# Performance work log

Hardware: AMD Instinct MI355X
Metric: run time of the kernel (lower is better)

## Reference

```python
import jax, jax.numpy as jnp
import numpy as np
import math

HIDDEN = 2048
HEADS = 16
HEAD_DIM = HIDDEN // HEADS
MAX_SEQ = 4096
ROPE_BASE = 10000.0


def rope_cos_sin(seq_len):
    # (seq_len, head_dim//2) angle table
    inv_freq = 1.0 / (ROPE_BASE ** (jnp.arange(0, HEAD_DIM, 2, dtype=jnp.float32) / HEAD_DIM))
    t = jnp.arange(seq_len, dtype=jnp.float32)
    ang = jnp.einsum('s,f->sf', t, inv_freq)
    return jnp.cos(ang), jnp.sin(ang)


def apply_rope(x, cos, sin):
    # x: (b, s, h, d); interleaved complex pairs along last dim
    b, s, h, d = x.shape
    xr = x.reshape(b, s, h, d // 2, 2)
    x0, x1 = xr[..., 0], xr[..., 1]
    c = cos[:s][None, :, None, :]
    sn = sin[:s][None, :, None, :]
    o0 = x0 * c - x1 * sn
    o1 = x0 * sn + x1 * c
    return jnp.stack([o0, o1], axis=-1).reshape(b, s, h, d)


def setup_inputs() -> dict:
    key = jax.random.key(0)
    k1, k2, k3, k4, k5, k6 = jax.random.split(key, 6)
    B, SQ, SK = 2, 2048, 2048
    x = jax.random.normal(k1, (B, SQ, HIDDEN), dtype=jnp.float32)
    enc = jax.random.normal(k2, (B, SK, HIDDEN), dtype=jnp.float32)
    mask = jnp.ones((B, SK), dtype=jnp.int32)
    scale = 0.02
    Wq = jax.random.normal(k3, (HIDDEN, HIDDEN), dtype=jnp.float32) * scale
    Wk = jax.random.normal(k4, (HIDDEN, HIDDEN), dtype=jnp.float32) * scale
    Wv = jax.random.normal(k5, (HIDDEN, HIDDEN), dtype=jnp.float32) * scale
    Wo = jax.random.normal(k6, (HIDDEN, HIDDEN), dtype=jnp.float32) * scale
    return {"x": x, "encoder_output": enc, "encoder_attention_mask": mask,
            "Wq": Wq, "Wk": Wk, "Wv": Wv, "Wo": Wo}


def reference(x, encoder_output, encoder_attention_mask, Wq, Wk, Wv, Wo):
    B, SQ, _ = x.shape
    SK = encoder_output.shape[1]
    # nn.Linear(bias=False): y = x @ W^T
    q = (x @ Wq.T).reshape(B, SQ, HEADS, HEAD_DIM)
    k = (encoder_output @ Wk.T).reshape(B, SK, HEADS, HEAD_DIM)
    v = (encoder_output @ Wv.T).reshape(B, SK, HEADS, HEAD_DIM)
    cos, sin = rope_cos_sin(max(SQ, SK))
    q = apply_rope(q, cos, sin)
    k = apply_rope(k, cos, sin)
    scale = math.sqrt(HEAD_DIM)
    # (b, h, sq, sk) scores
    scores = jnp.einsum('bqhd,bkhd->bhqk', q, k) / scale
    mask = encoder_attention_mask[:, None, None, :]
    scores = jnp.where(mask == 0, -jnp.inf, scores)
    attn = jax.nn.softmax(scores, axis=-1)
    out = jnp.einsum('bhqk,bkhd->bqhd', attn, v).reshape(B, SQ, HIDDEN)
    return out @ Wo.T
```

## Files before the change

### kernel.cpp

```cpp
#include <hip/hip_runtime.h>
#include <stdint.h>


#define LOG2E 1.44269504088896340736f
#define INV2PI 0.15915494309189535f

typedef __attribute__((ext_vector_type(8))) short bf16x8;
typedef __attribute__((ext_vector_type(8))) uint16_t u16x8;
typedef __attribute__((ext_vector_type(4))) uint16_t u16x4;
typedef __attribute__((ext_vector_type(4))) float f32x4;

__device__ __forceinline__ uint16_t f2bf(float f) {
  union { float f; uint32_t i; } v; v.f = f;
  uint32_t x = v.i;
  return (uint16_t)((x + 0x7fffu + ((x >> 16) & 1u)) >> 16);
}
__device__ __forceinline__ uint32_t f_as_u(float f) { union { float f; uint32_t u; } v; v.f = f; return v.u; }
__device__ __forceinline__ float u_as_f(uint32_t u) { union { uint32_t u; float f; } v; v.u = u; return v.f; }
__device__ __forceinline__ void glds16(const void* g, void* l) {
  __builtin_amdgcn_global_load_lds((const __attribute__((address_space(1))) void*)g,
                                   (__attribute__((address_space(3))) void*)l, 16, 0, 0);
}

__global__ __launch_bounds__(256) void convert_f32_bf16(const float* __restrict__ in,
                                                        uint16_t* __restrict__ out) {
  const long i = ((long)blockIdx.x * 256 + threadIdx.x) * 8;
  const f32x4 a = *(const f32x4*)(in + i);
  const f32x4 b = *(const f32x4*)(in + i + 4);
  u16x8 o;
#pragma unroll
  for (int j = 0; j < 4; ++j) { o[j] = f2bf(a[j]); o[4 + j] = f2bf(b[j]); }
  *(u16x8*)(out + i) = o;
}

__global__ __launch_bounds__(256) void mask_bias(const int* __restrict__ m,
                                                 float* __restrict__ bias) {
  const int i = blockIdx.x * 256 + threadIdx.x;
  bias[i] = m[i] ? 0.0f : -__builtin_inff();
}

#define EPI_ROPE 0
#define EPI_VT   1
#define EPI_F32  2

template <int MODE>
__global__ __launch_bounds__(256) void gemm_bt(const uint16_t* __restrict__ A,
                                               const uint16_t* __restrict__ W,
                                               void* __restrict__ Cv,
                                               int M, int N, int K, float oscale) {
  __shared__ __align__(16) uint16_t As[128 * 32];
  __shared__ __align__(16) uint16_t Bs[128 * 32];
  const int tid = threadIdx.x;
  const int lane = tid & 63;
  const int w = tid >> 6;
  const int r16 = lane & 15, quad = lane >> 4;
  const int m0 = blockIdx.y * 128, n0 = blockIdx.x * 128;
  const int wm = (w >> 1) * 64, wn = (w & 1) * 64;
  f32x4 acc[4][4] = {};
  const int srow = 32 * w + (lane >> 2);
  const int scol = (lane & 3) * 8;
  const uint16_t* Ag = A + (long)(m0 + srow) * K + scol;
  const uint16_t* Wg = W + (long)(n0 + srow) * K + scol;
  uint16_t* AsW = As + 2 * w * 512;
  uint16_t* BsW = Bs + 2 * w * 512;
  for (int k0 = 0; k0 < K; k0 += 32) {
    glds16(Ag + k0, AsW);
    glds16(Ag + k0 + (long)16 * K, AsW + 512);
    glds16(Wg + k0, BsW);
    glds16(Wg + k0 + (long)16 * K, BsW + 512);
    __syncthreads();
    bf16x8 af[4], bfr[4];
#pragma unroll
    for (int mt = 0; mt < 4; ++mt)
      af[mt] = *(const bf16x8*)(As + (wm + mt * 16 + r16) * 32 + quad * 8);
#pragma unroll
    for (int nt = 0; nt < 4; ++nt)
      bfr[nt] = *(const bf16x8*)(Bs + (wn + nt * 16 + r16) * 32 + quad * 8);
#pragma unroll
    for (int mt = 0; mt < 4; ++mt)
#pragma unroll
      for (int nt = 0; nt < 4; ++nt)
        acc[mt][nt] = __builtin_amdgcn_mfma_f32_16x16x32_bf16(af[mt], bfr[nt], acc[mt][nt], 0, 0, 0);
    __syncthreads();
  }

#pragma unroll
  for (int mt = 0; mt < 4; ++mt)
#pragma unroll
    for (int nt = 0; nt < 4; ++nt) {
      const int col = n0 + wn + nt * 16 + r16;
      const int rowbase = m0 + wm + mt * 16 + quad * 4;
      if constexpr (MODE == EPI_F32) {
        float* C = (float*)Cv;
#pragma unroll
        for (int r = 0; r < 4; ++r)
          C[(long)(rowbase + r) * N + col] = acc[mt][nt][r];
      } else if constexpr (MODE == EPI_ROPE) {
        uint16_t* C = (uint16_t*)Cv;
        const int f = (col >> 1) & 63;
        const float inv = __builtin_amdgcn_exp2f((float)f * (-13.287712379549449f / 64.0f));
        const float sgn = (col & 1) ? 1.0f : -1.0f;
#pragma unroll
        for (int r = 0; r < 4; ++r) {
          const float val = acc[mt][nt][r];
          const float partner = __shfl_xor(val, 1);
          const int s = (rowbase + r) & 2047;
          const float rev = __builtin_amdgcn_fractf((float)s * inv * INV2PI);
          const float sn = __builtin_amdgcn_sinf(rev);
          const float cs = __builtin_amdgcn_cosf(rev);
          C[(long)(rowbase + r) * N + col] = f2bf((val * cs + sgn * partner * sn) * oscale);
        }
      } else {
        uint16_t* Vt = (uint16_t*)Cv;
        const int h = col >> 7, d = col & 127;
        const int b = rowbase >> 11, s = rowbase & 2047;
        u16x4 pk;
#pragma unroll
        for (int r = 0; r < 4; ++r) pk[r] = f2bf(acc[mt][nt][r]);
        *(u16x4*)(Vt + (long)((b * 16 + h) * 128 + d) * 2048 + s) = pk;
      }
    }
}

__global__ __launch_bounds__(256) void attn_kernel(const uint16_t* __restrict__ Q,
                                                   const uint16_t* __restrict__ K,
                                                   const uint16_t* __restrict__ Vt,
                                                   const float* __restrict__ bias,
                                                   uint16_t* __restrict__ O) {
  __shared__ __align__(16) uint16_t Ks[2][32 * 128];
  __shared__ __align__(16) uint16_t Vts[2][128 * 32];
  __shared__ __align__(16) uint16_t Ps[4][32 * 40];
  const int tid = threadIdx.x;
  const int lane = tid & 63;
  const int w = tid >> 6;
  const int r16 = lane & 15, quad = lane >> 4;
  const int h = blockIdx.y, b = blockIdx.z;
  const int qbase = blockIdx.x * 128 + w * 32;

  bf16x8 qf[2][4];
#pragma unroll
  for (int t = 0; t < 2; ++t) {
    const uint16_t* qb = Q + ((long)(b * 2048 + qbase + t * 16 + r16)) * 2048 + h * 128 + quad * 8;
#pragma unroll
    for (int c = 0; c < 4; ++c) qf[t][c] = *(const bf16x8*)(qb + c * 32);
  }
  f32x4 oacc[2][8] = {};
  float li[2][4] = {};

  uint16_t* PsW = &Ps[w][0];
  const float* brow = bias + b * 2048;

  const int key0[2] = {8 * w + quad, 8 * w + 4 + quad};
  const uint16_t* kg[2];
  const uint16_t* vg[2];
#pragma unroll
  for (int i = 0; i < 2; ++i) {
    kg[i] = K + ((long)(b * 2048 + key0[i])) * 2048 + h * 128 + 8 * (r16 ^ ((4 * i + quad) & 7));
    const int dim = 32 * w + 16 * i + (lane >> 2);
    vg[i] = Vt + ((long)((b * 16 + h) * 128 + dim)) * 2048 + 8 * ((lane & 3) ^ ((lane >> 2) & 3));
  }

#pragma unroll
  for (int i = 0; i < 2; ++i) {
    glds16(kg[i], &Ks[0][(2 * w + i) * 512]);
    glds16(vg[i], &Vts[0][(2 * w + i) * 512]);
    kg[i] += 32 * 2048;
    vg[i] += 32;
  }
  float bn0 = brow[r16], bn1 = brow[16 + r16];

  auto body = [&](int k0, const uint16_t* Kc, const uint16_t* Vc,
                  uint16_t* Kn, uint16_t* Vn, bool pf) {
    __syncthreads();
    const float bc0 = bn0, bc1 = bn1;
    if (pf) {
#pragma unroll
      for (int i = 0; i < 2; ++i) {
        glds16(kg[i], Kn + (2 * w + i) * 512);
        glds16(vg[i], Vn + (2 * w + i) * 512);
        kg[i] += 32 * 2048;
        vg[i] += 32;
      }
      bn0 = brow[k0 + 32 + r16];
      bn1 = brow[k0 + 48 + r16];
    }
#pragma unroll
    for (int ct = 0; ct < 2; ++ct) {
      const int key = ct * 16 + r16;
      const int kb = key & 7;
      bf16x8 kf[4];
#pragma unroll
      for (int c = 0; c < 4; ++c)
        kf[c] = *(const bf16x8*)(Kc + key * 128 + ((4 * c + quad) ^ kb) * 8);
      const float bv = ct ? bc1 : bc0;
      const int pc = ct * 2 + (r16 >> 3);
#pragma unroll
      for (int t = 0; t < 2; ++t) {
        f32x4 s = {};
#pragma unroll
        for (int c = 0; c < 4; ++c)
          s = __builtin_amdgcn_mfma_f32_16x16x32_bf16(qf[t][c], kf[c], s, 0, 0, 0);
#pragma unroll
        for (int r = 0; r < 4; ++r) {
          const float p = __builtin_amdgcn_exp2f(s[r] + bv);
          const uint32_t pb = f_as_u(p) + 0x8000u;
          const int row = t * 16 + quad * 4 + r;
          PsW[row * 40 + ((pc ^ r) << 3) + (r16 & 7)] = (uint16_t)(pb >> 16);
          li[t][r] += u_as_f(pb & 0xffff0000u);
        }
      }
    }
    bf16x8 pa[2];
#pragma unroll
    for (int t = 0; t < 2; ++t)
      pa[t] = *(const bf16x8*)(PsW + (t * 16 + r16) * 40 + ((quad ^ (r16 & 3)) << 3));
#pragma unroll
    for (int nt = 0; nt < 8; ++nt) {
      const int dim = nt * 16 + r16;
      bf16x8 vf = *(const bf16x8*)(Vc + dim * 32 + ((quad ^ (dim & 3)) << 3));
#pragma unroll
      for (int t = 0; t < 2; ++t)
        oacc[t][nt] = __builtin_amdgcn_mfma_f32_16x16x32_bf16(pa[t], vf, oacc[t][nt], 0, 0, 0);
    }
  };

  for (int kt2 = 0; kt2 < 32; ++kt2) {
    body(64 * kt2,      &Ks[0][0], &Vts[0][0], &Ks[1][0], &Vts[1][0], true);
    body(64 * kt2 + 32, &Ks[1][0], &Vts[1][0], &Ks[0][0], &Vts[0][0], kt2 < 31);
  }

#pragma unroll
  for (int off = 1; off < 16; off <<= 1)
#pragma unroll
    for (int t = 0; t < 2; ++t)
#pragma unroll
      for (int r = 0; r < 4; ++r) li[t][r] += __shfl_xor(li[t][r], off);

#pragma unroll
  for (int t = 0; t < 2; ++t) {
    uint16_t* ob = O + ((long)(b * 2048 + qbase + t * 16)) * 2048 + h * 128;
    float inv_l[4];
#pragma unroll
    for (int r = 0; r < 4; ++r) inv_l[r] = 1.0f / li[t][r];
#pragma unroll
    for (int nt = 0; nt < 8; ++nt)
#pragma unroll
      for (int r = 0; r < 4; ++r)
        ob[(long)(quad * 4 + r) * 2048 + nt * 16 + r16] = f2bf(oacc[t][nt][r] * inv_l[r]);
  }
}

extern "C" void kernel_launch(void* const* d_in, const int* in_sizes, int n_in,
                              void* d_out, int out_size, void* d_ws, size_t ws_size,
                              hipStream_t stream) {
  const float* x   = (const float*)d_in[0];
  const float* enc = (const float*)d_in[1];
  const int*   msk = (const int*)d_in[2];
  const float* Wq  = (const float*)d_in[3];
  const float* Wk  = (const float*)d_in[4];
  const float* Wv  = (const float*)d_in[5];
  const float* Wo  = (const float*)d_in[6];
  float* out = (float*)d_out;

  const long NELT = 8L * 1024 * 1024;
  const long WELT = 4L * 1024 * 1024;
  uint16_t* Qb   = (uint16_t*)d_ws;
  uint16_t* Kb   = Qb + NELT;
  uint16_t* Vtb  = Kb + NELT;
  uint16_t* xb   = Vtb + NELT;
  uint16_t* encb = xb + NELT;
  uint16_t* Wb   = encb + NELT;
  uint16_t* Ob   = xb;
  float*    biasb = (float*)encb;

  const float cs_exp = 0.088388347648318447f * LOG2E;

  const dim3 gb(16, 32);
  const int CB_ACT = (int)(NELT / 2048);
  const int CB_W   = (int)(WELT / 2048);

  convert_f32_bf16<<<CB_ACT, 256, 0, stream>>>(x, xb);
  convert_f32_bf16<<<CB_W, 256, 0, stream>>>(Wq, Wb);
  gemm_bt<EPI_ROPE><<<gb, 256, 0, stream>>>(xb, Wb, Qb, 4096, 2048, 2048, cs_exp);

  convert_f32_bf16<<<CB_ACT, 256, 0, stream>>>(enc, encb);
  convert_f32_bf16<<<CB_W, 256, 0, stream>>>(Wk, Wb);
  gemm_bt<EPI_ROPE><<<gb, 256, 0, stream>>>(encb, Wb, Kb, 4096, 2048, 2048, 1.0f);

  convert_f32_bf16<<<CB_W, 256, 0, stream>>>(Wv, Wb);
  gemm_bt<EPI_VT><<<gb, 256, 0, stream>>>(encb, Wb, Vtb, 4096, 2048, 2048, 1.0f);

  mask_bias<<<16, 256, 0, stream>>>(msk, biasb);

  attn_kernel<<<dim3(16, 16, 2), 256, 0, stream>>>(Qb, Kb, Vtb, biasb, Ob);

  convert_f32_bf16<<<CB_W, 256, 0, stream>>>(Wo, Wb);
  gemm_bt<EPI_F32><<<gb, 256, 0, stream>>>(Ob, Wb, out, 4096, 2048, 2048, 1.0f);
}
```

Before: 489.0 us.

## Double-buffer GEMM LDS tiles and fuse K/V projections into one launch

The GEMM now double-buffers the shared-memory A/B tiles, issuing the next k-tile's global-to-LDS loads right after the barrier so they overlap the current MFMAs, and uses one barrier per step instead of two. The K and V projections are merged into a single launch over N=4096, with blocks picking the weight and epilogue (RoPE store or transposed V store) by column range. This cuts one launch and uses a larger grid. In exchange, LDS use doubles, which may lower occupancy, and the V weights reuse the x buffer.

```diff
diff --git a/kernel.cpp b/kernel.cpp
--- a/kernel.cpp
+++ b/kernel.cpp
@@ -40,16 +40,35 @@
 }
 
 #define EPI_ROPE 0
-#define EPI_VT   1
+#define EPI_KV   1
 #define EPI_F32  2
+
+__device__ __forceinline__ void epi_rope_store(uint16_t* C, const f32x4& a, int rowbase,
+                                               int col, int N, float oscale) {
+  const int f = (col >> 1) & 63;
+  const float inv = __builtin_amdgcn_exp2f((float)f * (-13.287712379549449f / 64.0f));
+  const float sgn = (col & 1) ? 1.0f : -1.0f;
+#pragma unroll
+  for (int r = 0; r < 4; ++r) {
+    const float val = a[r];
+    const float partner = __shfl_xor(val, 1);
+    const int s = (rowbase + r) & 2047;
+    const float rev = __builtin_amdgcn_fractf((float)s * inv * INV2PI);
+    const float sn = __builtin_amdgcn_sinf(rev);
+    const float cs = __builtin_amdgcn_cosf(rev);
+    C[(long)(rowbase + r) * N + col] = f2bf((val * cs + sgn * partner * sn) * oscale);
+  }
+}
 
 template <int MODE>
 __global__ __launch_bounds__(256) void gemm_bt(const uint16_t* __restrict__ A,
-                                               const uint16_t* __restrict__ W,
-                                               void* __restrict__ Cv,
+                                               const uint16_t* __restrict__ W0,
+                                               const uint16_t* __restrict__ W1,
+                                               void* __restrict__ C0v,
+                                               void* __restrict__ C1v,
                                                int M, int N, int K, float oscale) {
-  __shared__ __align__(16) uint16_t As[128 * 32];
-  __shared__ __align__(16) uint16_t Bs[128 * 32];
+  __shared__ __align__(16) uint16_t As[2][128 * 32];
+  __shared__ __align__(16) uint16_t Bs[2][128 * 32];
   const int tid = threadIdx.x;
   const int lane = tid & 63;
   const int w = tid >> 6;
@@ -59,29 +78,44 @@
   f32x4 acc[4][4] = {};
   const int srow = 32 * w + (lane >> 2);
   const int scol = (lane & 3) * 8;
+  const uint16_t* Wbase = (MODE == EPI_KV && n0 >= 2048) ? W1 + (long)(n0 - 2048) * K
+                                                         : W0 + (long)n0 * K;
   const uint16_t* Ag = A + (long)(m0 + srow) * K + scol;
-  const uint16_t* Wg = W + (long)(n0 + srow) * K + scol;
-  uint16_t* AsW = As + 2 * w * 512;
-  uint16_t* BsW = Bs + 2 * w * 512;
-  for (int k0 = 0; k0 < K; k0 += 32) {
-    glds16(Ag + k0, AsW);
-    glds16(Ag + k0 + (long)16 * K, AsW + 512);
-    glds16(Wg + k0, BsW);
-    glds16(Wg + k0 + (long)16 * K, BsW + 512);
+  const uint16_t* Wg = Wbase + (long)srow * K + scol;
+  const int co = 2 * w * 512;
+
+  glds16(Ag, &As[0][co]);
+  glds16(Ag + (long)16 * K, &As[0][co + 512]);
+  glds16(Wg, &Bs[0][co]);
+  glds16(Wg + (long)16 * K, &Bs[0][co + 512]);
+
+  auto body = [&](int k1, const uint16_t* Ac, const uint16_t* Bc,
+                  uint16_t* An, uint16_t* Bn, bool pf) {
     __syncthreads();
+    if (pf) {
+      glds16(Ag + k1, An + co);
+      glds16(Ag + k1 + (long)16 * K, An + co + 512);
+      glds16(Wg + k1, Bn + co);
+      glds16(Wg + k1 + (long)16 * K, Bn + co + 512);
+    }
     bf16x8 af[4], bfr[4];
 #pragma unroll
     for (int mt = 0; mt < 4; ++mt)
-      af[mt] = *(const bf16x8*)(As + (wm + mt * 16 + r16) * 32 + quad * 8);
+      af[mt] = *(const bf16x8*)(Ac + (wm + mt * 16 + r16) * 32 + quad * 8);
 #pragma unroll
     for (int nt = 0; nt < 4; ++nt)
-      bfr[nt] = *(const bf16x8*)(Bs + (wn + nt * 16 + r16) * 32 + quad * 8);
+      bfr[nt] = *(const bf16x8*)(Bc + (wn + nt * 16 + r16) * 32 + quad * 8);
 #pragma unroll
     for (int mt = 0; mt < 4; ++mt)
 #pragma unroll
       for (int nt = 0; nt < 4; ++nt)
         acc[mt][nt] = __builtin_amdgcn_mfma_f32_16x16x32_bf16(af[mt], bfr[nt], acc[mt][nt], 0, 0, 0);
-    __syncthreads();
+  };
+
+  const int NK2 = K >> 6;
+  for (int kk = 0; kk < NK2; ++kk) {
+    body((2 * kk + 1) * 32, &As[0][0], &Bs[0][0], &As[1][0], &Bs[1][0], true);
+    body((2 * kk + 2) * 32, &As[1][0], &Bs[1][0], &As[0][0], &Bs[0][0], kk < NK2 - 1);
   }
 
 #pragma unroll
@@ -91,33 +125,25 @@
       const int col = n0 + wn + nt * 16 + r16;
       const int rowbase = m0 + wm + mt * 16 + quad * 4;
       if constexpr (MODE == EPI_F32) {
-        float* C = (float*)Cv;
+        float* C = (float*)C0v;
 #pragma unroll
         for (int r = 0; r < 4; ++r)
           C[(long)(rowbase + r) * N + col] = acc[mt][nt][r];
       } else if constexpr (MODE == EPI_ROPE) {
-        uint16_t* C = (uint16_t*)Cv;
-        const int f = (col >> 1) & 63;
-        const float inv = __builtin_amdgcn_exp2f((float)f * (-13.287712379549449f / 64.0f));
-        const float sgn = (col & 1) ? 1.0f : -1.0f;
-#pragma unroll
-        for (int r = 0; r < 4; ++r) {
-          const float val = acc[mt][nt][r];
-          const float partner = __shfl_xor(val, 1);
-          const int s = (rowbase + r) & 2047;
-          const float rev = __builtin_amdgcn_fractf((float)s * inv * INV2PI);
-          const float sn = __builtin_amdgcn_sinf(rev);
-          const float cs = __builtin_amdgcn_cosf(rev);
-          C[(long)(rowbase + r) * N + col] = f2bf((val * cs + sgn * partner * sn) * oscale);
+        epi_rope_store((uint16_t*)C0v, acc[mt][nt], rowbase, col, N, oscale);
+      } else {
+        if (n0 < 2048) {
+          epi_rope_store((uint16_t*)C0v, acc[mt][nt], rowbase, col, 2048, 1.0f);
+        } else {
+          uint16_t* Vt = (uint16_t*)C1v;
+          const int c = col - 2048;
+          const int h = c >> 7, d = c & 127;
+          const int b = rowbase >> 11, s = rowbase & 2047;
+          u16x4 pk;
+#pragma unroll
+          for (int r = 0; r < 4; ++r) pk[r] = f2bf(acc[mt][nt][r]);
+          *(u16x4*)(Vt + (long)((b * 16 + h) * 128 + d) * 2048 + s) = pk;
         }
-      } else {
-        uint16_t* Vt = (uint16_t*)Cv;
-        const int h = col >> 7, d = col & 127;
-        const int b = rowbase >> 11, s = rowbase & 2047;
-        u16x4 pk;
-#pragma unroll
-        for (int r = 0; r < 4; ++r) pk[r] = f2bf(acc[mt][nt][r]);
-        *(u16x4*)(Vt + (long)((b * 16 + h) * 128 + d) * 2048 + s) = pk;
       }
     }
 }
@@ -270,30 +296,31 @@
   uint16_t* xb   = Vtb + NELT;
   uint16_t* encb = xb + NELT;
   uint16_t* Wb   = encb + NELT;
+  uint16_t* Wvb  = xb;
   uint16_t* Ob   = xb;
   float*    biasb = (float*)encb;
 
   const float cs_exp = 0.088388347648318447f * LOG2E;
 
-  const dim3 gb(16, 32);
   const int CB_ACT = (int)(NELT / 2048);
   const int CB_W   = (int)(WELT / 2048);
 
   convert_f32_bf16<<<CB_ACT, 256, 0, stream>>>(x, xb);
   convert_f32_bf16<<<CB_W, 256, 0, stream>>>(Wq, Wb);
-  gemm_bt<EPI_ROPE><<<gb, 256, 0, stream>>>(xb, Wb, Qb, 4096, 2048, 2048, cs_exp);
+  gemm_bt<EPI_ROPE><<<dim3(16, 32), 256, 0, stream>>>(xb, Wb, nullptr, Qb, nullptr,
+                                                      4096, 2048, 2048, cs_exp);
 
   convert_f32_bf16<<<CB_ACT, 256, 0, stream>>>(enc, encb);
   convert_f32_bf16<<<CB_W, 256, 0, stream>>>(Wk, Wb);
-  gemm_bt<EPI_ROPE><<<gb, 256, 0, stream>>>(encb, Wb, Kb, 4096, 2048, 2048, 1.0f);
-
-  convert_f32_bf16<<<CB_W, 256, 0, stream>>>(Wv, Wb);
-  gemm_bt<EPI_VT><<<gb, 256, 0, stream>>>(encb, Wb, Vtb, 4096, 2048, 2048, 1.0f);
+  convert_f32_bf16<<<CB_W, 256, 0, stream>>>(Wv, Wvb);
+  gemm_bt<EPI_KV><<<dim3(32, 32), 256, 0, stream>>>(encb, Wb, Wvb, Kb, Vtb,
+                                                    4096, 4096, 2048, 1.0f);
 
   mask_bias<<<16, 256, 0, stream>>>(msk, biasb);
 
   attn_kernel<<<dim3(16, 16, 2), 256, 0, stream>>>(Qb, Kb, Vtb, biasb, Ob);
 
   convert_f32_bf16<<<CB_W, 256, 0, stream>>>(Wo, Wb);
-  gemm_bt<EPI_F32><<<gb, 256, 0, stream>>>(Ob, Wb, out, 4096, 2048, 2048, 1.0f);
-}
+  gemm_bt<EPI_F32><<<dim3(16, 32), 256, 0, stream>>>(Ob, Wb, nullptr, out, nullptr,
+                                                     4096, 2048, 2048, 1.0f);
+}
```

New measurement: 484.5 us. No clear change (-0.9%).
